# Performance work log

Hardware: AMD Instinct MI355X
Metric: run time of the kernel (lower is better)

The kernel has to match this reference:

```python
import jax, jax.numpy as jnp
import numpy as np

B, N, FV_IN, FV_OUT, FE_IN, FE_OUT = 32, 128, 128, 128, 128, 128


def setup_inputs() -> dict:
    key = jax.random.key(0)
    ks = jax.random.split(key, 8)
    s = lambda fan_in: 1.0 / np.sqrt(fan_in)
    return {
        "v_in": jax.random.normal(ks[0], (B, N, FV_IN), dtype=jnp.float32),
        "e_in": jax.random.normal(ks[1], (B, N, N, FE_IN), dtype=jnp.float32),
        # e_vert_layer: Linear(vert_f_in, edge_f_out)
        "W_ev": jax.random.uniform(ks[2], (FV_IN, FE_OUT), jnp.float32, -s(FV_IN), s(FV_IN)),
        "b_ev": jax.random.uniform(ks[3], (FE_OUT,), jnp.float32, -s(FV_IN), s(FV_IN)),
        # e_layer: Linear(edge_f_in, edge_f_out)
        "W_e": jax.random.uniform(ks[4], (FE_IN, FE_OUT), jnp.float32, -s(FE_IN), s(FE_IN)),
        "b_e": jax.random.uniform(ks[5], (FE_OUT,), jnp.float32, -s(FE_IN), s(FE_IN)),
        # v_layer: Linear(vert_f_in + edge_f_out, vert_f_out)
        "W_v": jax.random.uniform(ks[6], (FV_IN + FE_OUT, FV_OUT), jnp.float32, -s(FV_IN + FE_OUT), s(FV_IN + FE_OUT)),
        "b_v": jax.random.uniform(ks[7], (FV_OUT,), jnp.float32, -s(FV_IN + FE_OUT), s(FV_IN + FE_OUT)),
    }


def reference(v_in, e_in, W_ev, b_ev, W_e, b_e, W_v, b_v):
    # per-vertex projection to edge feature space: [B, N, FE_OUT]
    e_v = jnp.einsum("bnf,fg->bng", v_in, W_ev) + b_ev
    # outer vertex sum broadcast: [B, N, N, FE_OUT]
    outer_v_sum = e_v[:, None, :, :] + e_v[:, :, None, :]
    # edge projection: [B, N, N, FE_OUT]
    e = jnp.einsum("bmnf,fg->bmng", e_in, W_e) + b_e
    e_out = jax.nn.relu(e + outer_v_sum)
    # sum-aggregate over dim 1 -> per-vertex edge summary [B, N, FE_OUT]
    per_v_e = jnp.sum(e_out, axis=1)
    vert_e_combined = jnp.concatenate([per_v_e, v_in], axis=2)
    v = jnp.einsum("bnf,fg->bng", vert_e_combined, W_v) + b_v
    v_out = jax.nn.relu(v)
    return (v_out, e_out)
```

## Files before the change

### kernel.cpp

```cpp
#include <hip/hip_runtime.h>
#include <cstdint>
#include <cstring>

#define B_ 32
#define N_ 128
#define F_ 128
#define SPLIT_ 4

typedef __attribute__((ext_vector_type(8))) __bf16 bf16x8;
typedef __attribute__((ext_vector_type(4))) float f32x4;

__device__ inline uint16_t f2bf_bits(float f) {
  __bf16 h = (__bf16)f;
  uint16_t u;
  __builtin_memcpy(&u, &h, 2);
  return u;
}

__device__ inline void gld16(const float* src, float* dst) {
  __builtin_amdgcn_global_load_lds(
      (const __attribute__((address_space(1))) unsigned int*)src,
      (__attribute__((address_space(3))) unsigned int*)dst, 16, 0, 0);
}

__global__ __launch_bounds__(128) void ev_kernel(const float* __restrict__ v_in,
                                                 const float* __restrict__ W_ev,
                                                 const float* __restrict__ b_ev,
                                                 float* __restrict__ e_v) {
  __shared__ float vr[8][F_];
  const int R0 = blockIdx.x * 8;
  const int tid = threadIdx.x;
#pragma unroll
  for (int i = 0; i < 8; ++i) vr[i][tid] = v_in[(size_t)(R0 + i) * F_ + tid];
  __syncthreads();
  float acc[8];
  const float bb = b_ev[tid];
#pragma unroll
  for (int i = 0; i < 8; ++i) acc[i] = bb;
  for (int f = 0; f < F_; ++f) {
    const float wv = W_ev[f * F_ + tid];
#pragma unroll
    for (int i = 0; i < 8; ++i) acc[i] += vr[i][f] * wv;
  }
#pragma unroll
  for (int i = 0; i < 8; ++i) e_v[(size_t)(R0 + i) * F_ + tid] = acc[i];
}

__global__ void pack_kernel(const float* __restrict__ W_e, uint32_t* __restrict__ wp) {
  const int idx = blockIdx.x * 256 + threadIdx.x;
  const int t = idx >> 6, l = idx & 63;
  const int kt = t >> 3, gt = t & 7;
  const int kbase = kt * 32 + ((l >> 4) << 3);
  const int g = gt * 16 + (l & 15);
#pragma unroll
  for (int p = 0; p < 4; ++p) {
    const uint32_t lo = f2bf_bits(W_e[(kbase + 2 * p) * F_ + g]);
    const uint32_t hi = f2bf_bits(W_e[(kbase + 2 * p + 1) * F_ + g]);
    wp[idx * 4 + p] = lo | (hi << 16);
  }
}

__global__ __launch_bounds__(512, 4) void main_kernel(
    const float* __restrict__ e_in, const float* __restrict__ e_v,
    const float* __restrict__ b_e, const bf16x8* __restrict__ wp,
    float* __restrict__ e_out, float* __restrict__ pve_part) {
  __shared__ __align__(16) float buf[2 * 2 * 2048];

  const int tid = threadIdx.x;
  const int w = tid >> 6, l = tid & 63;
  const int bid = blockIdx.x;
  const int s = bid & 3, nt = (bid >> 2) & 7, b = bid >> 5;
  const int n0 = nt * 16;
  const int lr = (l >> 4) << 2;
  const int lc = l & 15;
  const int ml = w & 1;
  const int gq = w >> 1;
  const int m0base = s * 32;

  bf16x8 wreg[4][2];
#pragma unroll
  for (int kt = 0; kt < 4; ++kt)
#pragma unroll
    for (int j = 0; j < 2; ++j)
      wreg[kt][j] = wp[(kt * 8 + gq * 2 + j) * 64 + l];

  f32x4 evn[2];
#pragma unroll
  for (int j = 0; j < 2; ++j) {
    const int g0 = (gq * 2 + j) * 16 + lr;
    evn[j] = *reinterpret_cast<const f32x4*>(&e_v[(size_t)(b * N_ + n0 + lc) * F_ + g0]) +
             *reinterpret_cast<const f32x4*>(&b_e[g0]);
  }

  f32x4 pve[2];
#pragma unroll
  for (int j = 0; j < 2; ++j) { pve[j][0] = 0.f; pve[j][1] = 0.f; pve[j][2] = 0.f; pve[j][3] = 0.f; }

  const int sw = w >> 2;
  const int ci = l & 31;
  const int rpar = l >> 5;
  const float* einb = e_in + (size_t)b * N_ * N_ * F_;

#define STAGE(pp, it2)                                                        \
  {                                                                           \
    const int m_ = m0base + (it2) * 2 + sw;                                   \
    const float* mb_ = einb + ((size_t)m_ * N_ + n0) * F_;                    \
    _Pragma("unroll") for (int j_ = 0; j_ < 2; ++j_) {                        \
      const int cc_ = ((w << 1) | j_) & 7;                                    \
      const int r_ = (cc_ << 1) | rpar;                                       \
      const int sc_ = ci ^ (r_ & 7);                                          \
      gld16(mb_ + r_ * F_ + sc_ * 4, &buf[(pp) * 4096 + sw * 2048 + (cc_ << 8)]); \
    }                                                                         \
  }

  STAGE(0, 0);

  const int swz = lc & 7;
  for (int it = 0; it < 16; ++it) {
    const int p = it & 1;
    __syncthreads();
    if (it < 15) STAGE(p ^ 1, it + 1);

    const int fbase = p * 4096 + ml * 2048 + lc * 128;
    f32x4 acc[2];
#pragma unroll
    for (int j = 0; j < 2; ++j) { acc[j][0] = 0.f; acc[j][1] = 0.f; acc[j][2] = 0.f; acc[j][3] = 0.f; }

#pragma unroll
    for (int kt = 0; kt < 4; ++kt) {
      const int cA = kt * 8 + ((l >> 4) << 1);
      const f32x4 f0 = *reinterpret_cast<const f32x4*>(&buf[fbase + ((cA ^ swz) << 2)]);
      const f32x4 f1 = *reinterpret_cast<const f32x4*>(&buf[fbase + (((cA + 1) ^ swz) << 2)]);
      bf16x8 a;
#pragma unroll
      for (int e = 0; e < 4; ++e) {
        a[e] = (__bf16)f0[e];
        a[e + 4] = (__bf16)f1[e];
      }
      acc[0] = __builtin_amdgcn_mfma_f32_16x16x32_bf16(wreg[kt][0], a, acc[0], 0, 0, 0);
      acc[1] = __builtin_amdgcn_mfma_f32_16x16x32_bf16(wreg[kt][1], a, acc[1], 0, 0, 0);
    }

    const int m = m0base + it * 2 + ml;
    const float* evm = &e_v[((size_t)b * N_ + m) * F_];
    float* op = e_out + (((size_t)(b * N_) + m) * N_ + n0 + lc) * F_;
#pragma unroll
    for (int j = 0; j < 2; ++j) {
      const int g0 = (gq * 2 + j) * 16 + lr;
      f32x4 v = acc[j] + evn[j] + *reinterpret_cast<const f32x4*>(&evm[g0]);
#pragma unroll
      for (int q = 0; q < 4; ++q) v[q] = fmaxf(v[q], 0.f);
      pve[j] += v;
      *reinterpret_cast<f32x4*>(&op[g0]) = v;
    }
  }

  __syncthreads();
  const int sbase = gq * 512 + lc * 32;
  if (ml == 0) {
#pragma unroll
    for (int j = 0; j < 2; ++j)
      *reinterpret_cast<f32x4*>(&buf[sbase + j * 16 + lr]) = pve[j];
  }
  __syncthreads();
  if (ml == 1) {
    float* pp = pve_part + (((size_t)s * B_ + b) * N_ + n0 + lc) * F_;
#pragma unroll
    for (int j = 0; j < 2; ++j) {
      const f32x4 sum = pve[j] + *reinterpret_cast<const f32x4*>(&buf[sbase + j * 16 + lr]);
      *reinterpret_cast<f32x4*>(&pp[(gq * 2 + j) * 16 + lr]) = sum;
    }
  }
#undef STAGE
}

__global__ __launch_bounds__(128) void v_kernel(
    const float* __restrict__ v_in, const float* __restrict__ pve_part,
    const float* __restrict__ W_v, const float* __restrict__ b_v,
    float* __restrict__ v_out) {
  __shared__ float rows[8][256];
  const int R0 = blockIdx.x * 8;
  const int tid = threadIdx.x;
#pragma unroll
  for (int i = 0; i < 8; ++i) {
    const size_t r = R0 + i;
    float acc = 0.f;
#pragma unroll
    for (int s = 0; s < SPLIT_; ++s)
      acc += pve_part[((size_t)s * B_ * N_ + r) * F_ + tid];
    rows[i][tid] = acc;
    rows[i][128 + tid] = v_in[r * F_ + tid];
  }
  __syncthreads();
  float acc[8];
  const float bb = b_v[tid];
#pragma unroll
  for (int i = 0; i < 8; ++i) acc[i] = bb;
  for (int f = 0; f < 256; ++f) {
    const float wv = W_v[f * F_ + tid];
#pragma unroll
    for (int i = 0; i < 8; ++i) acc[i] += rows[i][f] * wv;
  }
#pragma unroll
  for (int i = 0; i < 8; ++i)
    v_out[(size_t)(R0 + i) * F_ + tid] = fmaxf(acc[i], 0.f);
}

extern "C" void kernel_launch(void* const* d_in, const int* in_sizes, int n_in,
                              void* d_out, int out_size, void* d_ws, size_t ws_size,
                              hipStream_t stream) {
  const float* v_in = (const float*)d_in[0];
  const float* e_in = (const float*)d_in[1];
  const float* W_ev = (const float*)d_in[2];
  const float* b_ev = (const float*)d_in[3];
  const float* W_e  = (const float*)d_in[4];
  const float* b_e  = (const float*)d_in[5];
  const float* W_v  = (const float*)d_in[6];
  const float* b_v  = (const float*)d_in[7];

  float* out = (float*)d_out;
  float* v_out = out;
  float* e_out = out + (size_t)B_ * N_ * F_;

  char* ws = (char*)d_ws;
  float* e_v = (float*)ws;
  uint32_t* wpack = (uint32_t*)(ws + (size_t)2097152);
  float* pve_part = (float*)(ws + (size_t)2097152 + 65536);

  ev_kernel<<<(B_ * N_) / 8, 128, 0, stream>>>(v_in, W_ev, b_ev, e_v);
  pack_kernel<<<8, 256, 0, stream>>>(W_e, wpack);
  main_kernel<<<B_ * 8 * SPLIT_, 512, 0, stream>>>(e_in, e_v, b_e,
                                                   (const bf16x8*)wpack,
                                                   e_out, pve_part);
  v_kernel<<<(B_ * N_) / 8, 128, 0, stream>>>(v_in, pve_part, W_v, b_v, v_out);
}
```

Before: 157.9 us.

## Halve main kernel block size, each wave handles both rows with vmcnt-based pipelining

Shrinks the main kernel block from 512 to 256 threads, so each wave now computes both m rows per iteration. This removes the cross-wave LDS reduction of per-vertex partial sums at the end. The full __syncthreads is replaced by an explicit s_waitcnt vmcnt(4) plus s_barrier, letting the next tile's global->LDS loads stay in flight. It also prefetches e_v rows into registers before issuing the stage, and writes e_out with nontemporal stores to avoid polluting the cache. Fewer waves per block and the manual waitcnt counting trade occupancy and scheduling safety for fewer barriers and less LDS traffic.

Result: slower. 175.7 us (+11.3%).

```diff
diff --git a/kernel.cpp b/kernel.cpp
--- a/kernel.cpp
+++ b/kernel.cpp
@@ -21,6 +21,10 @@
   __builtin_amdgcn_global_load_lds(
       (const __attribute__((address_space(1))) unsigned int*)src,
       (__attribute__((address_space(3))) unsigned int*)dst, 16, 0, 0);
+}
+
+__device__ inline void nt_store4(float* p, f32x4 v) {
+  __builtin_nontemporal_store(v, reinterpret_cast<f32x4*>(p));
 }
 
 __global__ __launch_bounds__(128) void ev_kernel(const float* __restrict__ v_in,
@@ -60,11 +64,11 @@
   }
 }
 
-__global__ __launch_bounds__(512, 4) void main_kernel(
+__global__ __launch_bounds__(256, 4) void main_kernel(
     const float* __restrict__ e_in, const float* __restrict__ e_v,
     const float* __restrict__ b_e, const bf16x8* __restrict__ wp,
     float* __restrict__ e_out, float* __restrict__ pve_part) {
-  __shared__ __align__(16) float buf[2 * 2 * 2048];
+  __shared__ __align__(16) float buf[2 * 4096];
 
   const int tid = threadIdx.x;
   const int w = tid >> 6, l = tid & 63;
@@ -73,21 +77,19 @@
   const int n0 = nt * 16;
   const int lr = (l >> 4) << 2;
   const int lc = l & 15;
-  const int ml = w & 1;
-  const int gq = w >> 1;
-  const int m0base = s * 32;
+  const int m0 = s * 32;
 
   bf16x8 wreg[4][2];
 #pragma unroll
   for (int kt = 0; kt < 4; ++kt)
 #pragma unroll
     for (int j = 0; j < 2; ++j)
-      wreg[kt][j] = wp[(kt * 8 + gq * 2 + j) * 64 + l];
+      wreg[kt][j] = wp[(kt * 8 + w * 2 + j) * 64 + l];
 
   f32x4 evn[2];
 #pragma unroll
   for (int j = 0; j < 2; ++j) {
-    const int g0 = (gq * 2 + j) * 16 + lr;
+    const int g0 = (w * 2 + j) * 16 + lr;
     evn[j] = *reinterpret_cast<const f32x4*>(&e_v[(size_t)(b * N_ + n0 + lc) * F_ + g0]) +
              *reinterpret_cast<const f32x4*>(&b_e[g0]);
   }
@@ -96,82 +98,89 @@
 #pragma unroll
   for (int j = 0; j < 2; ++j) { pve[j][0] = 0.f; pve[j][1] = 0.f; pve[j][2] = 0.f; pve[j][3] = 0.f; }
 
-  const int sw = w >> 2;
-  const int ci = l & 31;
-  const int rpar = l >> 5;
   const float* einb = e_in + (size_t)b * N_ * N_ * F_;
-
-#define STAGE(pp, it2)                                                        \
-  {                                                                           \
-    const int m_ = m0base + (it2) * 2 + sw;                                   \
-    const float* mb_ = einb + ((size_t)m_ * N_ + n0) * F_;                    \
-    _Pragma("unroll") for (int j_ = 0; j_ < 2; ++j_) {                        \
-      const int cc_ = ((w << 1) | j_) & 7;                                    \
-      const int r_ = (cc_ << 1) | rpar;                                       \
-      const int sc_ = ci ^ (r_ & 7);                                          \
-      gld16(mb_ + r_ * F_ + sc_ * 4, &buf[(pp) * 4096 + sw * 2048 + (cc_ << 8)]); \
-    }                                                                         \
+  const float* evb = e_v + (size_t)b * N_ * F_;
+
+#define STAGE(pp, itn)                                                   \
+  {                                                                      \
+    _Pragma("unroll") for (int q_ = 0; q_ < 4; ++q_) {                   \
+      const int t_ = w * 4 + q_;                                         \
+      const int mj_ = t_ >> 3, k_ = t_ & 7;                              \
+      const int m_ = m0 + (itn) * 2 + mj_;                               \
+      const int r_ = k_ * 2 + (l >> 5);                                  \
+      const int c_ = (l & 31) ^ (r_ & 7);                                \
+      gld16(einb + ((size_t)m_ * N_ + n0 + r_) * F_ + c_ * 4,            \
+            &buf[(pp) * 4096 + t_ * 256]);                               \
+    }                                                                    \
   }
 
   STAGE(0, 0);
 
-  const int swz = lc & 7;
   for (int it = 0; it < 16; ++it) {
     const int p = it & 1;
-    __syncthreads();
+    if (it == 0) {
+      asm volatile("s_waitcnt vmcnt(0)" ::: "memory");
+    } else {
+      asm volatile("s_waitcnt vmcnt(4)" ::: "memory");
+    }
+    __builtin_amdgcn_s_barrier();
+
+    const int mA = m0 + it * 2, mB = mA + 1;
+    f32x4 evmA[2], evmB[2];
+#pragma unroll
+    for (int j = 0; j < 2; ++j) {
+      const int g0 = (w * 2 + j) * 16 + lr;
+      evmA[j] = *reinterpret_cast<const f32x4*>(&evb[(size_t)mA * F_ + g0]);
+      evmB[j] = *reinterpret_cast<const f32x4*>(&evb[(size_t)mB * F_ + g0]);
+    }
+    __builtin_amdgcn_sched_barrier(0);
+
     if (it < 15) STAGE(p ^ 1, it + 1);
-
-    const int fbase = p * 4096 + ml * 2048 + lc * 128;
-    f32x4 acc[2];
-#pragma unroll
-    for (int j = 0; j < 2; ++j) { acc[j][0] = 0.f; acc[j][1] = 0.f; acc[j][2] = 0.f; acc[j][3] = 0.f; }
-
-#pragma unroll
-    for (int kt = 0; kt < 4; ++kt) {
-      const int cA = kt * 8 + ((l >> 4) << 1);
-      const f32x4 f0 = *reinterpret_cast<const f32x4*>(&buf[fbase + ((cA ^ swz) << 2)]);
-      const f32x4 f1 = *reinterpret_cast<const f32x4*>(&buf[fbase + (((cA + 1) ^ swz) << 2)]);
-      bf16x8 a;
-#pragma unroll
-      for (int e = 0; e < 4; ++e) {
-        a[e] = (__bf16)f0[e];
-        a[e + 4] = (__bf16)f1[e];
+    __builtin_amdgcn_sched_barrier(0);
+
+#pragma unroll
+    for (int mj = 0; mj < 2; ++mj) {
+      const int fb = p * 4096 + mj * 2048;
+      f32x4 acc[2];
+#pragma unroll
+      for (int j = 0; j < 2; ++j) { acc[j][0] = 0.f; acc[j][1] = 0.f; acc[j][2] = 0.f; acc[j][3] = 0.f; }
+
+#pragma unroll
+      for (int kt = 0; kt < 4; ++kt) {
+        const int cA = kt * 8 + ((l >> 4) << 1);
+        const f32x4 f0 = *reinterpret_cast<const f32x4*>(
+            &buf[fb + lc * 128 + ((cA ^ (lc & 7)) << 2)]);
+        const f32x4 f1 = *reinterpret_cast<const f32x4*>(
+            &buf[fb + lc * 128 + (((cA + 1) ^ (lc & 7)) << 2)]);
+        bf16x8 a;
+#pragma unroll
+        for (int e = 0; e < 4; ++e) {
+          a[e] = (__bf16)f0[e];
+          a[e + 4] = (__bf16)f1[e];
+        }
+        acc[0] = __builtin_amdgcn_mfma_f32_16x16x32_bf16(wreg[kt][0], a, acc[0], 0, 0, 0);
+        acc[1] = __builtin_amdgcn_mfma_f32_16x16x32_bf16(wreg[kt][1], a, acc[1], 0, 0, 0);
       }
-      acc[0] = __builtin_amdgcn_mfma_f32_16x16x32_bf16(wreg[kt][0], a, acc[0], 0, 0, 0);
-      acc[1] = __builtin_amdgcn_mfma_f32_16x16x32_bf16(wreg[kt][1], a, acc[1], 0, 0, 0);
+
+      const int m = mj ? mB : mA;
+      float* op = e_out + (((size_t)(b * N_) + m) * N_ + n0 + lc) * F_;
+#pragma unroll
+      for (int j = 0; j < 2; ++j) {
+        const int g0 = (w * 2 + j) * 16 + lr;
+        f32x4 v = acc[j] + evn[j] + (mj ? evmB[j] : evmA[j]);
+#pragma unroll
+        for (int q = 0; q < 4; ++q) v[q] = fmaxf(v[q], 0.f);
+        pve[j] += v;
+        nt_store4(&op[g0], v);
+      }
     }
-
-    const int m = m0base + it * 2 + ml;
-    const float* evm = &e_v[((size_t)b * N_ + m) * F_];
-    float* op = e_out + (((size_t)(b * N_) + m) * N_ + n0 + lc) * F_;
-#pragma unroll
-    for (int j = 0; j < 2; ++j) {
-      const int g0 = (gq * 2 + j) * 16 + lr;
-      f32x4 v = acc[j] + evn[j] + *reinterpret_cast<const f32x4*>(&evm[g0]);
-#pragma unroll
-      for (int q = 0; q < 4; ++q) v[q] = fmaxf(v[q], 0.f);
-      pve[j] += v;
-      *reinterpret_cast<f32x4*>(&op[g0]) = v;
-    }
-  }
-
-  __syncthreads();
-  const int sbase = gq * 512 + lc * 32;
-  if (ml == 0) {
-#pragma unroll
-    for (int j = 0; j < 2; ++j)
-      *reinterpret_cast<f32x4*>(&buf[sbase + j * 16 + lr]) = pve[j];
-  }
-  __syncthreads();
-  if (ml == 1) {
-    float* pp = pve_part + (((size_t)s * B_ + b) * N_ + n0 + lc) * F_;
-#pragma unroll
-    for (int j = 0; j < 2; ++j) {
-      const f32x4 sum = pve[j] + *reinterpret_cast<const f32x4*>(&buf[sbase + j * 16 + lr]);
-      *reinterpret_cast<f32x4*>(&pp[(gq * 2 + j) * 16 + lr]) = sum;
-    }
   }
 #undef STAGE
+
+  float* pp = pve_part + (((size_t)s * B_ + b) * N_ + n0 + lc) * F_;
+#pragma unroll
+  for (int j = 0; j < 2; ++j)
+    *reinterpret_cast<f32x4*>(&pp[(w * 2 + j) * 16 + lr]) = pve[j];
 }
 
 __global__ __launch_bounds__(128) void v_kernel(
@@ -229,7 +238,7 @@
 
   ev_kernel<<<(B_ * N_) / 8, 128, 0, stream>>>(v_in, W_ev, b_ev, e_v);
   pack_kernel<<<8, 256, 0, stream>>>(W_e, wpack);
-  main_kernel<<<B_ * 8 * SPLIT_, 512, 0, stream>>>(e_in, e_v, b_e,
+  main_kernel<<<B_ * 8 * SPLIT_, 256, 0, stream>>>(e_in, e_v, b_e,
                                                    (const bf16x8*)wpack,
                                                    e_out, pve_part);
   v_kernel<<<(B_ * N_) / 8, 128, 0, stream>>>(v_in, pve_part, W_v, b_v, v_out);
```

## Triple-buffer e_in staging with vmcnt waits and stage e_v rows in LDS

Applied to the files above, without the earlier changes.

Replaces the double-buffered LDS staging of e_in with a three-deep ring, prefetching two stages ahead. The per-iteration __syncthreads is replaced by explicit s_waitcnt vmcnt counts plus a raw s_barrier, so the next tiles' loads stay in flight while the current tile is processed. The 32 per-block e_v rows are loaded once into LDS instead of being read from global memory every iteration. The trade-off is a doubling of LDS per block (about 64KB), which likely limits how many 512-thread blocks fit per CU. The hand-tuned vmcnt values also depend on the exact number and order of outstanding loads and stores.

New measurement: 162.2 us. 1.03x slower.

```diff
diff --git a/kernel.cpp b/kernel.cpp
--- a/kernel.cpp
+++ b/kernel.cpp
@@ -64,7 +64,8 @@
     const float* __restrict__ e_in, const float* __restrict__ e_v,
     const float* __restrict__ b_e, const bf16x8* __restrict__ wp,
     float* __restrict__ e_out, float* __restrict__ pve_part) {
-  __shared__ __align__(16) float buf[2 * 2 * 2048];
+  __shared__ __align__(16) float buf[3 * 4096];
+  __shared__ __align__(16) float evlds[32 * F_];
 
   const int tid = threadIdx.x;
   const int w = tid >> 6, l = tid & 63;
@@ -75,7 +76,7 @@
   const int lc = l & 15;
   const int ml = w & 1;
   const int gq = w >> 1;
-  const int m0base = s * 32;
+  const int m0 = s * 32;
 
   bf16x8 wreg[4][2];
 #pragma unroll
@@ -96,32 +97,49 @@
 #pragma unroll
   for (int j = 0; j < 2; ++j) { pve[j][0] = 0.f; pve[j][1] = 0.f; pve[j][2] = 0.f; pve[j][3] = 0.f; }
 
-  const int sw = w >> 2;
-  const int ci = l & 31;
-  const int rpar = l >> 5;
   const float* einb = e_in + (size_t)b * N_ * N_ * F_;
-
-#define STAGE(pp, it2)                                                        \
-  {                                                                           \
-    const int m_ = m0base + (it2) * 2 + sw;                                   \
-    const float* mb_ = einb + ((size_t)m_ * N_ + n0) * F_;                    \
-    _Pragma("unroll") for (int j_ = 0; j_ < 2; ++j_) {                        \
-      const int cc_ = ((w << 1) | j_) & 7;                                    \
-      const int r_ = (cc_ << 1) | rpar;                                       \
-      const int sc_ = ci ^ (r_ & 7);                                          \
-      gld16(mb_ + r_ * F_ + sc_ * 4, &buf[(pp) * 4096 + sw * 2048 + (cc_ << 8)]); \
-    }                                                                         \
+  const float* evb = e_v + (size_t)b * N_ * F_;
+
+#pragma unroll
+  for (int q = 0; q < 2; ++q) {
+    const int row0 = w * 4 + q * 2;
+    gld16(evb + (size_t)(m0 + row0 + (l >> 5)) * F_ + (l & 31) * 4,
+          &evlds[row0 * F_]);
+  }
+
+#define STAGE(q3, itn)                                                   \
+  {                                                                      \
+    _Pragma("unroll") for (int q_ = 0; q_ < 2; ++q_) {                   \
+      const int t_ = w * 2 + q_;                                         \
+      const int mj_ = t_ >> 3, k_ = t_ & 7;                              \
+      const int m_ = m0 + (itn) * 2 + mj_;                               \
+      const int r_ = k_ * 2 + (l >> 5);                                  \
+      const int c_ = (l & 31) ^ (r_ & 7);                                \
+      gld16(einb + ((size_t)m_ * N_ + n0 + r_) * F_ + c_ * 4,            \
+            &buf[(q3) * 4096 + mj_ * 2048 + k_ * 256]);                  \
+    }                                                                    \
   }
 
   STAGE(0, 0);
+  STAGE(1, 1);
 
   const int swz = lc & 7;
   for (int it = 0; it < 16; ++it) {
-    const int p = it & 1;
-    __syncthreads();
-    if (it < 15) STAGE(p ^ 1, it + 1);
-
-    const int fbase = p * 4096 + ml * 2048 + lc * 128;
+    const int q3 = it % 3;
+    if (it == 0) {
+      asm volatile("s_waitcnt vmcnt(2)" ::: "memory");
+    } else if (it == 1 || it == 15) {
+      asm volatile("s_waitcnt vmcnt(4)" ::: "memory");
+    } else {
+      asm volatile("s_waitcnt vmcnt(6)" ::: "memory");
+    }
+    __builtin_amdgcn_sched_barrier(0);
+    __builtin_amdgcn_s_barrier();
+    __builtin_amdgcn_sched_barrier(0);
+
+    if (it < 14) STAGE((it + 2) % 3, it + 2);
+
+    const int fb = q3 * 4096 + ml * 2048;
     f32x4 acc[2];
 #pragma unroll
     for (int j = 0; j < 2; ++j) { acc[j][0] = 0.f; acc[j][1] = 0.f; acc[j][2] = 0.f; acc[j][3] = 0.f; }
@@ -129,8 +147,10 @@
 #pragma unroll
     for (int kt = 0; kt < 4; ++kt) {
       const int cA = kt * 8 + ((l >> 4) << 1);
-      const f32x4 f0 = *reinterpret_cast<const f32x4*>(&buf[fbase + ((cA ^ swz) << 2)]);
-      const f32x4 f1 = *reinterpret_cast<const f32x4*>(&buf[fbase + (((cA + 1) ^ swz) << 2)]);
+      const f32x4 f0 = *reinterpret_cast<const f32x4*>(
+          &buf[fb + lc * 128 + ((cA ^ swz) << 2)]);
+      const f32x4 f1 = *reinterpret_cast<const f32x4*>(
+          &buf[fb + lc * 128 + (((cA + 1) ^ swz) << 2)]);
       bf16x8 a;
 #pragma unroll
       for (int e = 0; e < 4; ++e) {
@@ -141,19 +161,20 @@
       acc[1] = __builtin_amdgcn_mfma_f32_16x16x32_bf16(wreg[kt][1], a, acc[1], 0, 0, 0);
     }
 
-    const int m = m0base + it * 2 + ml;
-    const float* evm = &e_v[((size_t)b * N_ + m) * F_];
+    const int m = m0 + it * 2 + ml;
+    const float* evmrow = &evlds[(it * 2 + ml) * F_];
     float* op = e_out + (((size_t)(b * N_) + m) * N_ + n0 + lc) * F_;
 #pragma unroll
     for (int j = 0; j < 2; ++j) {
       const int g0 = (gq * 2 + j) * 16 + lr;
-      f32x4 v = acc[j] + evn[j] + *reinterpret_cast<const f32x4*>(&evm[g0]);
+      f32x4 v = acc[j] + evn[j] + *reinterpret_cast<const f32x4*>(&evmrow[g0]);
 #pragma unroll
       for (int q = 0; q < 4; ++q) v[q] = fmaxf(v[q], 0.f);
       pve[j] += v;
       *reinterpret_cast<f32x4*>(&op[g0]) = v;
     }
   }
+#undef STAGE
 
   __syncthreads();
   const int sbase = gq * 512 + lc * 32;
@@ -171,7 +192,6 @@
       *reinterpret_cast<f32x4*>(&pp[(gq * 2 + j) * 16 + lr]) = sum;
     }
   }
-#undef STAGE
 }
 
 __global__ __launch_bounds__(128) void v_kernel(
```
